# Performance work log

Measured on AMD Instinct MI355X. Metric: run time of the kernel, lower is better.

## Reference

```python
import jax, jax.numpy as jnp
import numpy as np

HIDDEN = 1024
HEADS = 16
HEAD_DIM = HIDDEN // HEADS
EPS = 1e-5


def setup_inputs() -> dict:
    key = jax.random.key(0)
    ks = jax.random.split(key, 12)
    B, S, H = 2, 2048, HIDDEN
    s = 1.0 / np.sqrt(H)
    x = jax.random.normal(ks[0], (B, S, H), dtype=jnp.float32)
    Wq = jax.random.normal(ks[1], (H, H), dtype=jnp.float32) * s
    bq = jnp.zeros((H,), dtype=jnp.float32)
    Wk = jax.random.normal(ks[2], (H, H), dtype=jnp.float32) * s
    bk = jnp.zeros((H,), dtype=jnp.float32)
    Wv = jax.random.normal(ks[3], (H, H), dtype=jnp.float32) * s
    bv = jnp.zeros((H,), dtype=jnp.float32)
    Wg = jax.random.normal(ks[4], (2 * H, H), dtype=jnp.float32) * (1.0 / np.sqrt(2 * H))
    bg = jnp.zeros((H,), dtype=jnp.float32)
    gamma = jnp.ones((H,), dtype=jnp.float32)
    beta = jnp.zeros((H,), dtype=jnp.float32)
    return {"x": x, "Wq": Wq, "bq": bq, "Wk": Wk, "bk": bk, "Wv": Wv, "bv": bv,
            "Wg": Wg, "bg": bg, "gamma": gamma, "beta": beta}


def reference(x, Wq, bq, Wk, bk, Wv, bv, Wg, bg, gamma, beta):
    B, S, H = x.shape
    def heads(t):  # [B,S,H] -> [B,nH,S,hd]
        return t.reshape(B, S, HEADS, HEAD_DIM).transpose(0, 2, 1, 3)
    Q = heads(x @ Wq + bq)
    K = heads(x @ Wk + bk)
    V = heads(x @ Wv + bv)
    scores = jnp.einsum('bhqd,bhkd->bhqk', Q, K) / jnp.sqrt(jnp.float32(HEAD_DIM))
    flow = scores - scores.transpose(0, 1, 3, 2)  # antisymmetric
    w = jax.nn.softmax(flow, axis=-1)
    flowed = jnp.einsum('bhqk,bhkd->bhqd', w, V)
    flowed = flowed.transpose(0, 2, 1, 3).reshape(B, S, H)
    gate = jax.nn.sigmoid(jnp.concatenate([x, flowed], axis=-1) @ Wg + bg)
    y = x + gate * flowed
    mu = jnp.mean(y, axis=-1, keepdims=True)
    var = jnp.mean(jnp.square(y - mu), axis=-1, keepdims=True)
    return (y - mu) * jax.lax.rsqrt(var + EPS) * gamma + beta
```

## Files before the change

### kernel.cpp

```cpp
#include <hip/hip_runtime.h>
#include <hip/hip_bf16.h>

#define S_LEN 2048
#define NHEAD 16
#define HDIM 64
#define HID 1024

typedef __attribute__((ext_vector_type(8))) short bf16x8;
typedef __attribute__((ext_vector_type(4))) float f32x4;
typedef __attribute__((ext_vector_type(4))) unsigned int u32x4;
typedef __attribute__((ext_vector_type(2))) unsigned int u32x2;

__device__ __forceinline__ unsigned short f2bf(float x) {
    unsigned int u = __builtin_bit_cast(unsigned int, x);
    u = (u + 0x7fffu + ((u >> 16) & 1u)) >> 16;
    return (unsigned short)u;
}
__device__ __forceinline__ float bf2f(unsigned short s) {
    unsigned int u = ((unsigned int)s) << 16;
    return __builtin_bit_cast(float, u);
}
__device__ __forceinline__ unsigned cvtpk_bf16(float lo, float hi) {
    unsigned r;
    asm("v_cvt_pk_bf16_f32 %0, %1, %2" : "=v"(r) : "v"(lo), "v"(hi));
    return r;
}
__device__ __forceinline__ void gload16(const short* g, short* l) {
    __builtin_amdgcn_global_load_lds(
        (const __attribute__((address_space(1))) unsigned int*)g,
        (__attribute__((address_space(3))) unsigned int*)l, 16, 0, 0);
}
__device__ __forceinline__ bf16x8 negbf8(bf16x8 v) {
    u32x4 u = __builtin_bit_cast(u32x4, v);
    #pragma unroll
    for (int e = 0; e < 4; e++) u[e] ^= 0x80008000u;
    return __builtin_bit_cast(bf16x8, u);
}

#define QSCALE 0.1803368801111168f

__global__ void cvt_kernel(const float* __restrict__ src, short* __restrict__ dst, int n4) {
    int i = blockIdx.x * blockDim.x + threadIdx.x;
    if (i < n4) {
        float4 v = reinterpret_cast<const float4*>(src)[i];
        short4 o;
        o.x = (short)f2bf(v.x); o.y = (short)f2bf(v.y);
        o.z = (short)f2bf(v.z); o.w = (short)f2bf(v.w);
        reinterpret_cast<short4*>(dst)[i] = o;
    }
}

__global__ void transpose_all(const float* __restrict__ Wq, const float* __restrict__ Wk,
                              const float* __restrict__ Wv, const float* __restrict__ Wg,
                              short* __restrict__ WT, short* __restrict__ WgT) {
    __shared__ float tile[32][33];
    int z = blockIdx.z;
    const float* src; short* dst; int R;
    if (z == 0)      { src = Wq; dst = WT;               R = 1024; }
    else if (z == 1) { src = Wk; dst = WT + 1024 * 1024; R = 1024; }
    else if (z == 2) { src = Wv; dst = WT + 2 * 1024 * 1024; R = 1024; }
    else             { src = Wg; dst = WgT;              R = 2048; }
    int by = blockIdx.y * 32;
    if (by >= R) return;
    int bx = blockIdx.x * 32;
    const int C = 1024;
    int tx = threadIdx.x, ty = threadIdx.y;
    #pragma unroll
    for (int i = ty; i < 32; i += 8)
        tile[i][tx] = src[(size_t)(by + i) * C + bx + tx];
    __syncthreads();
    #pragma unroll
    for (int i = ty; i < 32; i += 8)
        dst[(size_t)(bx + i) * R + by + tx] = (short)f2bf(tile[tx][i]);
}

__global__ void vtrans_kernel(const short* __restrict__ Vb, short* __restrict__ VT) {
    __shared__ short tile[32][34];
    int s0 = blockIdx.x * 32;
    int dv0 = blockIdx.y * 32;
    int bh = blockIdx.z;
    int b = bh >> 4, h = bh & 15;
    int tx = threadIdx.x, ty = threadIdx.y;
    #pragma unroll
    for (int i = ty; i < 32; i += 8)
        tile[i][tx] = Vb[(size_t)(b * S_LEN + s0 + i) * HID + h * HDIM + dv0 + tx];
    __syncthreads();
    #pragma unroll
    for (int i = ty; i < 32; i += 8)
        VT[(size_t)(bh * HDIM + dv0 + i) * S_LEN + s0 + tx] = tile[tx][i];
}

__global__ __launch_bounds__(256, 2)
void gemm_qkv(const short* __restrict__ xb, const short* __restrict__ WT,
              const float* __restrict__ bq, const float* __restrict__ bk,
              const float* __restrict__ bv,
              short* __restrict__ Qb, short* __restrict__ Kb, short* __restrict__ Vb) {
    __shared__ short Al[2][128 * 32];
    __shared__ short Bl[2][128 * 32];
    int lin = blockIdx.x + 32 * blockIdx.y;
    int nid = (lin & 7) * 96 + (lin >> 3);
    int mb = nid & 31, nb = nid >> 5;
    int tid = threadIdx.x;
    int wave = tid >> 6, lane = tid & 63;
    int wm = wave >> 1, wn = wave & 1;
    int lr = lane & 15, lg = lane >> 4;

    int r = tid >> 2;
    int c = tid & 3;
    int sc = (c ^ (r & 3)) * 8;
    int dst0 = tid * 8;
    int dst1 = (tid + 256) * 8;
    const short* a0 = xb + (size_t)(mb * 128 + r) * 1024 + sc;
    const short* a1 = a0 + (size_t)64 * 1024;
    const short* b0 = WT + (size_t)(nb * 128 + r) * 1024 + sc;
    const short* b1 = b0 + (size_t)64 * 1024;
    int fsw = (lg ^ (lr & 3)) * 8;

    f32x4 acc[4][4] = {};

    for (int ks = 0; ks < 16; ++ks) {
        int kg = ks * 64;
        __syncthreads();
        gload16(a0 + kg,      &Al[0][dst0]);
        gload16(a1 + kg,      &Al[0][dst1]);
        gload16(a0 + kg + 32, &Al[1][dst0]);
        gload16(a1 + kg + 32, &Al[1][dst1]);
        gload16(b0 + kg,      &Bl[0][dst0]);
        gload16(b1 + kg,      &Bl[0][dst1]);
        gload16(b0 + kg + 32, &Bl[1][dst0]);
        gload16(b1 + kg + 32, &Bl[1][dst1]);
        __syncthreads();
        #pragma unroll
        for (int s = 0; s < 2; s++) {
            bf16x8 af[4], bfr[4];
            #pragma unroll
            for (int t = 0; t < 4; t++)
                af[t] = *(bf16x8*)&Al[s][(wm * 64 + t * 16 + lr) * 32 + fsw];
            #pragma unroll
            for (int t = 0; t < 4; t++)
                bfr[t] = *(bf16x8*)&Bl[s][(wn * 64 + t * 16 + lr) * 32 + fsw];
            #pragma unroll
            for (int i = 0; i < 4; i++)
                #pragma unroll
                for (int jn = 0; jn < 4; jn++)
                    acc[i][jn] = __builtin_amdgcn_mfma_f32_16x16x32_bf16(af[i], bfr[jn], acc[i][jn], 0, 0, 0);
        }
    }

    #pragma unroll
    for (int jn = 0; jn < 4; jn++) {
        int n = nb * 128 + wn * 64 + jn * 16 + lr;
        int which = n >> 10;
        int n1 = n & 1023;
        const float* bias = (which == 0) ? bq : (which == 1) ? bk : bv;
        short* out = (which == 0) ? Qb : (which == 1) ? Kb : Vb;
        float scale = (which == 0) ? QSCALE : 1.0f;
        float bv_ = bias[n1];
        #pragma unroll
        for (int i = 0; i < 4; i++) {
            #pragma unroll
            for (int j = 0; j < 4; j++) {
                int mm = mb * 128 + wm * 64 + i * 16 + lg * 4 + j;
                out[(size_t)mm * 1024 + n1] = (short)f2bf((acc[i][jn][j] + bv_) * scale);
            }
        }
    }
}

__global__ __launch_bounds__(256, 4)
void attn_kernel(const short* __restrict__ Qb, const short* __restrict__ Kb,
                 const short* __restrict__ VT, short* __restrict__ Fb) {
    __shared__ short Kt[64 * 64];
    __shared__ short Qt[64 * 64];
    __shared__ short Vt[64 * 64];
    __shared__ short Pl[4][16 * 64];

    int bid = (blockIdx.x & 7) * 128 + (blockIdx.x >> 3);
    int qb = bid & 31;
    int bh = bid >> 5;
    int b = bh >> 4, h = bh & 15;
    int tid = threadIdx.x;
    int wave = tid >> 6, lane = tid & 63;
    int lr = lane & 15, lg = lane >> 4;

    size_t rowbase = ((size_t)(b * S_LEN + qb * 64 + wave * 16 + lr)) * HID + h * HDIM;
    bf16x8 Qf[2], Kf[2];
    #pragma unroll
    for (int cc = 0; cc < 2; cc++) {
        Qf[cc] = *(const bf16x8*)(Qb + rowbase + cc * 32 + lg * 8);
        Kf[cc] = negbf8(*(const bf16x8*)(Kb + rowbase + cc * 32 + lg * 8));
    }

    int r0 = tid >> 3;
    int c = tid & 7;
    int swz = (c ^ (r0 & 7)) * 8;
    int dst0 = r0 * 64 + swz;
    int dst1 = (r0 + 32) * 64 + swz;
    const short* kp = Kb + (size_t)(b * S_LEN + r0) * HID + h * HDIM + c * 8;
    const short* qp = Qb + (size_t)(b * S_LEN + r0) * HID + h * HDIM + c * 8;
    const short* vp = VT + (size_t)bh * HDIM * S_LEN + (size_t)r0 * S_LEN + c * 8;

    bf16x8 kv0 = *(const bf16x8*)kp;
    bf16x8 kv1 = *(const bf16x8*)(kp + 32 * HID);
    bf16x8 qv0 = *(const bf16x8*)qp;
    bf16x8 qv1 = *(const bf16x8*)(qp + 32 * HID);
    bf16x8 vv0 = *(const bf16x8*)vp;
    bf16x8 vv1 = *(const bf16x8*)(vp + 32 * S_LEN);
    kp += 64 * HID; qp += 64 * HID; vp += 64;

    f32x4 O[4] = {};
    float m = -1e30f, l = 0.f;

    for (int kt = 0; kt < 32; ++kt) {
        __syncthreads();
        *(bf16x8*)&Kt[dst0] = kv0;
        *(bf16x8*)&Kt[dst1] = kv1;
        *(bf16x8*)&Qt[dst0] = qv0;
        *(bf16x8*)&Qt[dst1] = qv1;
        *(bf16x8*)&Vt[dst0] = vv0;
        *(bf16x8*)&Vt[dst1] = vv1;
        __syncthreads();

        if (kt < 31) {
            kv0 = *(const bf16x8*)kp;
            kv1 = *(const bf16x8*)(kp + 32 * HID);
            qv0 = *(const bf16x8*)qp;
            qv1 = *(const bf16x8*)(qp + 32 * HID);
            vv0 = *(const bf16x8*)vp;
            vv1 = *(const bf16x8*)(vp + 32 * S_LEN);
            kp += 64 * HID; qp += 64 * HID; vp += 64;
        }

        f32x4 S[4] = {};
        __builtin_amdgcn_s_setprio(1);
        #pragma unroll
        for (int t = 0; t < 4; t++) {
            #pragma unroll
            for (int c2 = 0; c2 < 2; c2++) {
                int fo = (t * 16 + lr) * 64 + (((4 * c2 + lg) ^ (lr & 7)) * 8);
                bf16x8 kf = *(bf16x8*)&Kt[fo];
                bf16x8 qf = *(bf16x8*)&Qt[fo];
                S[t] = __builtin_amdgcn_mfma_f32_16x16x32_bf16(kf, Qf[c2], S[t], 0, 0, 0);
                S[t] = __builtin_amdgcn_mfma_f32_16x16x32_bf16(qf, Kf[c2], S[t], 0, 0, 0);
            }
        }
        __builtin_amdgcn_s_setprio(0);

        float pm = -1e30f;
        #pragma unroll
        for (int t = 0; t < 4; t++)
            #pragma unroll
            for (int j = 0; j < 4; j++) pm = fmaxf(pm, S[t][j]);
        pm = fmaxf(pm, __shfl_xor(pm, 16));
        pm = fmaxf(pm, __shfl_xor(pm, 32));

        if (__any(pm > m + 8.f)) {
            float mn = fmaxf(m, pm);
            float alpha = exp2f(m - mn);
            m = mn;
            l *= alpha;
            float a[4];
            #pragma unroll
            for (int j = 0; j < 4; j++) a[j] = __shfl(alpha, lg * 4 + j);
            #pragma unroll
            for (int dvt = 0; dvt < 4; dvt++)
                #pragma unroll
                for (int j = 0; j < 4; j++) O[dvt][j] *= a[j];
        }

        unsigned Pd[4][2];
        float rs = 0.f;
        #pragma unroll
        for (int t = 0; t < 4; t++) {
            float p0 = exp2f(S[t][0] - m);
            float p1 = exp2f(S[t][1] - m);
            float p2 = exp2f(S[t][2] - m);
            float p3 = exp2f(S[t][3] - m);
            rs += (p0 + p1) + (p2 + p3);
            Pd[t][0] = cvtpk_bf16(p0, p1);
            Pd[t][1] = cvtpk_bf16(p2, p3);
        }
        rs += __shfl_xor(rs, 16);
        rs += __shfl_xor(rs, 32);
        l += rs;
        #pragma unroll
        for (int t = 0; t < 4; t++) {
            u32x2 pw;
            pw[0] = Pd[t][0];
            pw[1] = Pd[t][1];
            int po = lr * 64 + (((2 * t + (lg >> 1)) ^ (lr & 7)) * 8) + (lg & 1) * 4;
            *(u32x2*)&Pl[wave][po] = pw;
        }

        __builtin_amdgcn_s_setprio(1);
        #pragma unroll
        for (int c2 = 0; c2 < 2; c2++) {
            bf16x8 pf = *(bf16x8*)&Pl[wave][lr * 64 + (((4 * c2 + lg) ^ (lr & 7)) * 8)];
            #pragma unroll
            for (int dvt = 0; dvt < 4; dvt++) {
                bf16x8 vf = *(bf16x8*)&Vt[(dvt * 16 + lr) * 64 + (((4 * c2 + lg) ^ (lr & 7)) * 8)];
                O[dvt] = __builtin_amdgcn_mfma_f32_16x16x32_bf16(pf, vf, O[dvt], 0, 0, 0);
            }
        }
        __builtin_amdgcn_s_setprio(0);
    }

    float linv = 1.f / l;
    float li[4];
    #pragma unroll
    for (int j = 0; j < 4; j++) li[j] = __shfl(linv, lg * 4 + j);
    #pragma unroll
    for (int dvt = 0; dvt < 4; dvt++) {
        #pragma unroll
        for (int j = 0; j < 4; j++) {
            int q = qb * 64 + wave * 16 + lg * 4 + j;
            int dv = dvt * 16 + lr;
            Fb[((size_t)(b * S_LEN + q)) * HID + h * HDIM + dv] =
                (short)f2bf(O[dvt][j] * li[j]);
        }
    }
}

__global__ __launch_bounds__(256, 4)
void gemm_gate(const short* __restrict__ xb, const short* __restrict__ fb,
               const short* __restrict__ WgT, const float* __restrict__ bg,
               const float* __restrict__ x, float* __restrict__ y) {
    __shared__ short Al[2][64 * 32];
    __shared__ short Bl[2][64 * 32];
    int lin = blockIdx.x + 64 * blockIdx.y;
    int nid = (lin & 7) * 128 + (lin >> 3);
    int mb = nid & 63, nb = nid >> 6;
    int tid = threadIdx.x;
    int wave = tid >> 6, lane = tid & 63;
    int wm = wave >> 1, wn = wave & 1;
    int lr = lane & 15, lg = lane >> 4;

    int r = tid >> 2;
    int c = tid & 3;
    int sc = (c ^ (r & 3)) * 8;
    int dst0 = tid * 8;
    size_t arow = (size_t)(mb * 64 + r) * 1024 + sc;
    const short* b0 = WgT + (size_t)(nb * 64 + r) * 2048 + sc;
    int fsw = (lg ^ (lr & 3)) * 8;

    f32x4 acc[2][2] = {};

    for (int ks = 0; ks < 32; ++ks) {
        int kg = ks * 64;
        const short* A = (kg < 1024) ? (xb + kg) : (fb + (kg - 1024));
        __syncthreads();
        gload16(A + arow, &Al[0][dst0]);
        gload16(A + arow + 32, &Al[1][dst0]);
        gload16(b0 + kg, &Bl[0][dst0]);
        gload16(b0 + kg + 32, &Bl[1][dst0]);
        __syncthreads();
        bf16x8 af[2][2], bfr[2][2];
        #pragma unroll
        for (int t = 0; t < 2; t++)
            #pragma unroll
            for (int s = 0; s < 2; s++) {
                af[t][s]  = *(bf16x8*)&Al[s][(wm * 32 + t * 16 + lr) * 32 + fsw];
                bfr[t][s] = *(bf16x8*)&Bl[s][(wn * 32 + t * 16 + lr) * 32 + fsw];
            }
        #pragma unroll
        for (int i = 0; i < 2; i++)
            #pragma unroll
            for (int jn = 0; jn < 2; jn++)
                #pragma unroll
                for (int s = 0; s < 2; s++)
                    acc[i][jn] = __builtin_amdgcn_mfma_f32_16x16x32_bf16(af[i][s], bfr[jn][s], acc[i][jn], 0, 0, 0);
    }

    #pragma unroll
    for (int jn = 0; jn < 2; jn++) {
        int n = nb * 64 + wn * 32 + jn * 16 + lr;
        float bgv = bg[n];
        #pragma unroll
        for (int i = 0; i < 2; i++) {
            #pragma unroll
            for (int j = 0; j < 4; j++) {
                int mm = mb * 64 + wm * 32 + i * 16 + lg * 4 + j;
                size_t idx = (size_t)mm * 1024 + n;
                float z = acc[i][jn][j] + bgv;
                float gate = 1.f / (1.f + __expf(-z));
                float fv = bf2f((unsigned short)fb[idx]);
                y[idx] = x[idx] + gate * fv;
            }
        }
    }
}

__global__ __launch_bounds__(256)
void ln_kernel(float* __restrict__ y, const float* __restrict__ gamma,
               const float* __restrict__ beta) {
    int row = blockIdx.x;
    int tid = threadIdx.x;
    float4 v4 = *(const float4*)&y[(size_t)row * 1024 + tid * 4];
    float v[4] = {v4.x, v4.y, v4.z, v4.w};
    float s = v[0] + v[1] + v[2] + v[3];
    float s2 = v[0]*v[0] + v[1]*v[1] + v[2]*v[2] + v[3]*v[3];
    #pragma unroll
    for (int off = 1; off < 64; off <<= 1) {
        s += __shfl_xor(s, off);
        s2 += __shfl_xor(s2, off);
    }
    __shared__ float red[8];
    int wave = tid >> 6, lane = tid & 63;
    if (lane == 0) { red[wave] = s; red[4 + wave] = s2; }
    __syncthreads();
    s = red[0] + red[1] + red[2] + red[3];
    s2 = red[4] + red[5] + red[6] + red[7];
    float mu = s * (1.f / 1024.f);
    float var = s2 * (1.f / 1024.f) - mu * mu;
    float rsq = rsqrtf(var + 1e-5f);
    float4 o4;
    float* o = (float*)&o4;
    #pragma unroll
    for (int e = 0; e < 4; e++) {
        int n = tid * 4 + e;
        o[e] = (v[e] - mu) * rsq * gamma[n] + beta[n];
    }
    *(float4*)&y[(size_t)row * 1024 + tid * 4] = o4;
}

extern "C" void kernel_launch(void* const* d_in, const int* in_sizes, int n_in,
                              void* d_out, int out_size, void* d_ws, size_t ws_size,
                              hipStream_t stream) {
    const float* x     = (const float*)d_in[0];
    const float* Wq    = (const float*)d_in[1];
    const float* bq    = (const float*)d_in[2];
    const float* Wk    = (const float*)d_in[3];
    const float* bk    = (const float*)d_in[4];
    const float* Wv    = (const float*)d_in[5];
    const float* bv    = (const float*)d_in[6];
    const float* Wg    = (const float*)d_in[7];
    const float* bg    = (const float*)d_in[8];
    const float* gamma = (const float*)d_in[9];
    const float* beta  = (const float*)d_in[10];
    float* out = (float*)d_out;

    char* w = (char*)d_ws;
    const size_t MB = 1024 * 1024;
    short* xb  = (short*)(w + 0 * MB);
    short* Qb  = (short*)(w + 8 * MB);
    short* Kb  = (short*)(w + 16 * MB);
    short* Vb  = (short*)(w + 24 * MB);
    short* WT  = (short*)(w + 32 * MB);
    short* WgT = (short*)(w + 38 * MB);
    short* fb  = (short*)(w + 42 * MB);
    short* VT  = (short*)(w + 50 * MB);

    cvt_kernel<<<4096, 256, 0, stream>>>(x, xb, 4096 * 1024 / 4);
    dim3 tb(32, 8);
    transpose_all<<<dim3(32, 64, 4), tb, 0, stream>>>(Wq, Wk, Wv, Wg, WT, WgT);
    gemm_qkv<<<dim3(32, 24), 256, 0, stream>>>(xb, WT, bq, bk, bv, Qb, Kb, Vb);
    vtrans_kernel<<<dim3(64, 2, 32), tb, 0, stream>>>(Vb, VT);
    attn_kernel<<<1024, 256, 0, stream>>>(Qb, Kb, VT, fb);
    gemm_gate<<<dim3(64, 16), 256, 0, stream>>>(xb, fb, WgT, bg, x, out);
    ln_kernel<<<4096, 256, 0, stream>>>(out, gamma, beta);
}
```

Baseline: 180.8 us.

## Fuse V transpose into QKV GEMM epilogue and drop block swizzle

```diff
diff --git a/kernel.cpp b/kernel.cpp
--- a/kernel.cpp
+++ b/kernel.cpp
@@ -74,32 +74,14 @@
         dst[(size_t)(bx + i) * R + by + tx] = (short)f2bf(tile[tx][i]);
 }
 
-__global__ void vtrans_kernel(const short* __restrict__ Vb, short* __restrict__ VT) {
-    __shared__ short tile[32][34];
-    int s0 = blockIdx.x * 32;
-    int dv0 = blockIdx.y * 32;
-    int bh = blockIdx.z;
-    int b = bh >> 4, h = bh & 15;
-    int tx = threadIdx.x, ty = threadIdx.y;
-    #pragma unroll
-    for (int i = ty; i < 32; i += 8)
-        tile[i][tx] = Vb[(size_t)(b * S_LEN + s0 + i) * HID + h * HDIM + dv0 + tx];
-    __syncthreads();
-    #pragma unroll
-    for (int i = ty; i < 32; i += 8)
-        VT[(size_t)(bh * HDIM + dv0 + i) * S_LEN + s0 + tx] = tile[tx][i];
-}
-
 __global__ __launch_bounds__(256, 2)
 void gemm_qkv(const short* __restrict__ xb, const short* __restrict__ WT,
               const float* __restrict__ bq, const float* __restrict__ bk,
               const float* __restrict__ bv,
-              short* __restrict__ Qb, short* __restrict__ Kb, short* __restrict__ Vb) {
+              short* __restrict__ Qb, short* __restrict__ Kb, short* __restrict__ VT) {
     __shared__ short Al[2][128 * 32];
     __shared__ short Bl[2][128 * 32];
-    int lin = blockIdx.x + 32 * blockIdx.y;
-    int nid = (lin & 7) * 96 + (lin >> 3);
-    int mb = nid & 31, nb = nid >> 5;
+    int mb = blockIdx.x, nb = blockIdx.y;
     int tid = threadIdx.x;
     int wave = tid >> 6, lane = tid & 63;
     int wm = wave >> 1, wn = wave & 1;
@@ -147,21 +129,37 @@
         }
     }
 
+    int which = (nb * 128) >> 10;
     #pragma unroll
     for (int jn = 0; jn < 4; jn++) {
         int n = nb * 128 + wn * 64 + jn * 16 + lr;
-        int which = n >> 10;
         int n1 = n & 1023;
-        const float* bias = (which == 0) ? bq : (which == 1) ? bk : bv;
-        short* out = (which == 0) ? Qb : (which == 1) ? Kb : Vb;
-        float scale = (which == 0) ? QSCALE : 1.0f;
-        float bv_ = bias[n1];
-        #pragma unroll
-        for (int i = 0; i < 4; i++) {
-            #pragma unroll
-            for (int j = 0; j < 4; j++) {
-                int mm = mb * 128 + wm * 64 + i * 16 + lg * 4 + j;
-                out[(size_t)mm * 1024 + n1] = (short)f2bf((acc[i][jn][j] + bv_) * scale);
+        if (which < 2) {
+            const float* bias = (which == 0) ? bq : bk;
+            short* out = (which == 0) ? Qb : Kb;
+            float scale = (which == 0) ? QSCALE : 1.0f;
+            float bv_ = bias[n1];
+            #pragma unroll
+            for (int i = 0; i < 4; i++) {
+                #pragma unroll
+                for (int j = 0; j < 4; j++) {
+                    int mm = mb * 128 + wm * 64 + i * 16 + lg * 4 + j;
+                    out[(size_t)mm * 1024 + n1] = (short)f2bf(acc[i][jn][j] * scale + bv_ * scale);
+                }
+            }
+        } else {
+            int h = n1 >> 6, dv = n1 & 63;
+            float bv_ = bv[n1];
+            #pragma unroll
+            for (int i = 0; i < 4; i++) {
+                int mm0 = mb * 128 + wm * 64 + i * 16 + lg * 4;
+                int bb = mm0 >> 11, ss = mm0 & 2047;
+                short4 vvv;
+                vvv.x = (short)f2bf(acc[i][jn][0] + bv_);
+                vvv.y = (short)f2bf(acc[i][jn][1] + bv_);
+                vvv.z = (short)f2bf(acc[i][jn][2] + bv_);
+                vvv.w = (short)f2bf(acc[i][jn][3] + bv_);
+                *(short4*)&VT[((size_t)((bb * 16 + h) * 64 + dv)) * S_LEN + ss] = vvv;
             }
         }
     }
@@ -327,9 +325,7 @@
                const float* __restrict__ x, float* __restrict__ y) {
     __shared__ short Al[2][64 * 32];
     __shared__ short Bl[2][64 * 32];
-    int lin = blockIdx.x + 64 * blockIdx.y;
-    int nid = (lin & 7) * 128 + (lin >> 3);
-    int mb = nid & 63, nb = nid >> 6;
+    int mb = blockIdx.x, nb = blockIdx.y;
     int tid = threadIdx.x;
     int wave = tid >> 6, lane = tid & 63;
     int wm = wave >> 1, wn = wave & 1;
@@ -444,7 +440,6 @@
     short* xb  = (short*)(w + 0 * MB);
     short* Qb  = (short*)(w + 8 * MB);
     short* Kb  = (short*)(w + 16 * MB);
-    short* Vb  = (short*)(w + 24 * MB);
     short* WT  = (short*)(w + 32 * MB);
     short* WgT = (short*)(w + 38 * MB);
     short* fb  = (short*)(w + 42 * MB);
@@ -453,8 +448,7 @@
     cvt_kernel<<<4096, 256, 0, stream>>>(x, xb, 4096 * 1024 / 4);
     dim3 tb(32, 8);
     transpose_all<<<dim3(32, 64, 4), tb, 0, stream>>>(Wq, Wk, Wv, Wg, WT, WgT);
-    gemm_qkv<<<dim3(32, 24), 256, 0, stream>>>(xb, WT, bq, bk, bv, Qb, Kb, Vb);
-    vtrans_kernel<<<dim3(64, 2, 32), tb, 0, stream>>>(Vb, VT);
+    gemm_qkv<<<dim3(32, 24), 256, 0, stream>>>(xb, WT, bq, bk, bv, Qb, Kb, VT);
     attn_kernel<<<1024, 256, 0, stream>>>(Qb, Kb, VT, fb);
     gemm_gate<<<dim3(64, 16), 256, 0, stream>>>(xb, fb, WgT, bg, x, out);
     ln_kernel<<<4096, 256, 0, stream>>>(out, gamma, beta);
```

Result: faster. 171.3 us, median of 3 (-5.3%).
